# Optimization experiments

Measured on AMD Instinct MI355X. Metric: run time of the kernel, lower is better.

Reference implementation:

```python
import jax, jax.numpy as jnp
import numpy as np

B_SZ, T, H, N, L = 4, 512, 256, 64, 4
EPS = 1e-5

def _hippo(n):
    i = np.arange(n)[:, None]; j = np.arange(n)[None, :]
    A = np.where(i >= j, ((-1.0) ** (i - j)) * np.sqrt((2 * i + 1.0) * (2 * j + 1.0)), 0.0)
    # scale to be contractive so the 512-step dense recurrence stays finite
    A = A / (1.1 * np.linalg.norm(A, 2))
    return A.astype(np.float32)

def _xavier(key, shape):
    fan_in, fan_out = shape[1], shape[0]
    a = float(np.sqrt(6.0 / (fan_in + fan_out)))
    return jax.random.uniform(key, shape, jnp.float32, -a, a)

def setup_inputs() -> dict:
    key = jax.random.key(0)
    ks = jax.random.split(key, 8)
    x = jax.random.normal(ks[0], (B_SZ, T, H), jnp.float32)
    A = jnp.broadcast_to(jnp.asarray(_hippo(N)), (L, N, N))
    Bm = jnp.stack([_xavier(jax.random.fold_in(ks[1], l), (N, H)) for l in range(L)])
    Cm = jnp.stack([_xavier(jax.random.fold_in(ks[2], l), (H, N)) for l in range(L)])
    Dm = jnp.stack([_xavier(jax.random.fold_in(ks[3], l), (H, H)) for l in range(L)])
    Win = _xavier(ks[4], (H, H)); bin_ = jnp.zeros((H,), jnp.float32)
    Wout = _xavier(ks[5], (H, H)); bout = jnp.zeros((H,), jnp.float32)
    return {"x": x, "Win": Win, "bin_": bin_, "Wout": Wout, "bout": bout,
            "A": A, "Bm": Bm, "Cm": Cm, "Dm": Dm}

def _ln(x):
    m = jnp.mean(x, -1, keepdims=True)
    v = jnp.mean((x - m) ** 2, -1, keepdims=True)
    return (x - m) / jnp.sqrt(v + EPS)

def _ssm_layer(h, A, B, C, D):
    # h: (B,T,H); dense state (B,N,H)
    Cbar = C.mean(0)            # mean over output rows (matches C_state.mean(dim=2))
    BT = B.T                    # (H,N)
    DT = D.T                    # (H,H)
    def step(state, u):        # state (B,N,H), u (B,H)
        y = jnp.einsum('bnh,n->bh', state, Cbar) + u @ DT   # output uses pre-update state
        new_state = jnp.einsum('nm,bmh->bnh', A, state) + (u @ BT)[:, :, None]
        return new_state, y
    state0 = jnp.zeros((h.shape[0], A.shape[0], h.shape[2]), h.dtype)
    _, ys = jax.lax.scan(step, state0, jnp.swapaxes(h, 0, 1))  # scan over T
    y = jnp.swapaxes(ys, 0, 1)
    y = jax.nn.gelu(y, approximate=False) + h   # GELU -> (dropout=0) -> residual
    return _ln(y)

def reference(x, Win, bin_, Wout, bout, A, Bm, Cm, Dm):
    h = x @ Win.T + bin_
    for l in range(L):
        h = _ssm_layer(h, A[l], Bm[l], Cm[l], Dm[l])
    h = _ln(h)
    return h @ Wout.T + bout
```

## Files before the change

kernel.cpp:

```cpp
#include <hip/hip_runtime.h>

#define TSEQ 512
#define HDIM 256
#define NDIM 64
#define LC   48
#define MT   16
#define NWB  128

typedef __attribute__((ext_vector_type(4))) float  f32x4;
typedef __attribute__((ext_vector_type(8))) short  s16x8;
typedef __attribute__((ext_vector_type(4))) unsigned short u16x4;
typedef unsigned long long u64;
typedef unsigned short us;

#define MFMA16 __builtin_amdgcn_mfma_f32_16x16x32_bf16

__device__ __forceinline__ float lane_bcast(float v, int l) {
    return __int_as_float(__builtin_amdgcn_readlane(__float_as_int(v), l));
}
__device__ __forceinline__ us f2bf(float f) {
    unsigned u = __float_as_uint(f);
    u += 0x7fffu + ((u >> 16) & 1u);
    return (us)(u >> 16);
}
__device__ __forceinline__ float bf2f(us h) {
    return __uint_as_float(((unsigned)h) << 16);
}
__device__ __forceinline__ int swz(int row, int chunk) {
    return row * 512 + (((chunk) ^ (row & 7)) << 4);
}
__device__ __forceinline__ void st_mall(float* p, float v) {
    __hip_atomic_store(p, v, __ATOMIC_RELAXED, __HIP_MEMORY_SCOPE_AGENT);
}
__device__ __forceinline__ void st_mall8(u64* p, u64 v) {
    __hip_atomic_store(p, v, __ATOMIC_RELAXED, __HIP_MEMORY_SCOPE_AGENT);
}
__device__ __forceinline__ u64 ld_mall8(const u64* p) {
    return __hip_atomic_load(p, __ATOMIC_RELAXED, __HIP_MEMORY_SCOPE_AGENT);
}
__device__ __forceinline__ void flag_set(unsigned* f) {
    __hip_atomic_store(f, 1u, __ATOMIC_RELAXED, __HIP_MEMORY_SCOPE_AGENT);
}
__device__ __forceinline__ void flag_wait(const unsigned* f) {
    while (__hip_atomic_load(f, __ATOMIC_RELAXED, __HIP_MEMORY_SCOPE_AGENT) == 0u)
        __builtin_amdgcn_s_sleep(4);
}

__global__ void __launch_bounds__(512, 2) k_fused(
    const float* __restrict__ x, const float* __restrict__ bin,
    const float* __restrict__ bout, const float* __restrict__ A,
    const float* __restrict__ Bm, const float* __restrict__ Cm,
    const float* __restrict__ Dm, const float* __restrict__ Win,
    const float* __restrict__ Wout,
    us* __restrict__ Win_bf, us* __restrict__ Wout_bf,
    us* __restrict__ Bm_bf, us* __restrict__ Dm_bf,
    float* __restrict__ wbuf, float* __restrict__ BiA, float* __restrict__ BiB,
    unsigned* __restrict__ flags, float* __restrict__ out)
{
    __shared__ __align__(16) char smem[53568];
    us*    xl   = (us*)smem;
    float* yl   = (float*)(smem + 8192);
    float* bwin = (float*)(smem + 24832);
    float* wlds = (float*)(smem + 41216);
    float* cfin = (float*)(smem + 53504);

    const int gid = blockIdx.x, tid = threadIdx.x;
    const int lane = tid & 63, wv = tid >> 6;
    const int m = lane & 15, cgq = lane >> 4;
    const f32x4 z4 = {0.f, 0.f, 0.f, 0.f};
    unsigned* ctr = &flags[516];

    if (gid == NWB) {
        float* As  = (float*)smem;
        float* A8s = (float*)(smem + 16384);
        float* uls = (float*)(smem + 32768);
        float cbv = 0.f;
        if (wv < 4) {
            const float* cp = Cm + (size_t)wv * HDIM * NDIM + lane;
            float s0 = 0.f, s1 = 0.f, s2 = 0.f, s3 = 0.f;
            for (int h = 0; h < HDIM; h += 4) {
                s0 += cp[(h + 0) * NDIM]; s1 += cp[(h + 1) * NDIM];
                s2 += cp[(h + 2) * NDIM]; s3 += cp[(h + 3) * NDIM];
            }
            cbv = ((s0 + s1) + (s2 + s3)) * (1.0f / HDIM);
        } else {
            int t = tid - 256;
            for (int q = t; q < 1024; q += 256) ((f32x4*)As)[q] = ((const f32x4*)A)[q];
        }
        __syncthreads();
        if (wv < 4) {
            float u = cbv;
            uls[(wv * 8 + 0) * 64 + lane] = u;
#pragma unroll 1
            for (int s = 1; s < 8; ++s) {
                float p0 = 0.f, p1 = 0.f, p2 = 0.f, p3 = 0.f;
#pragma unroll
                for (int k = 0; k < 64; k += 4) {
                    p0 += As[(k + 0) * 64 + lane] * lane_bcast(u, k + 0);
                    p1 += As[(k + 1) * 64 + lane] * lane_bcast(u, k + 1);
                    p2 += As[(k + 2) * 64 + lane] * lane_bcast(u, k + 2);
                    p3 += As[(k + 3) * 64 + lane] * lane_bcast(u, k + 3);
                }
                u = (p0 + p1) + (p2 + p3);
                uls[(wv * 8 + s) * 64 + lane] = u;
            }
        } else {
            int t = tid - 256;
            int r = t >> 2, c0 = (t & 3) * 16;
            f32x4 a0 = z4, a1 = z4, a2 = z4, a3 = z4;
            for (int k = 0; k < 64; ++k) {
                float av = As[r * 64 + k];
                const f32x4* bp = (const f32x4*)(As + k * 64 + c0);
                a0 += av * bp[0]; a1 += av * bp[1]; a2 += av * bp[2]; a3 += av * bp[3];
            }
            f32x4* dp = (f32x4*)(A8s + r * 64 + c0);
            dp[0] = a0; dp[1] = a1; dp[2] = a2; dp[3] = a3;
        }
        __syncthreads();
        {
            int r = tid >> 3, c0 = (tid & 7) * 8;
            f32x4 a0 = z4, a1 = z4;
            for (int k = 0; k < 64; ++k) {
                float av = A8s[r * 64 + k];
                const f32x4* bp = (const f32x4*)(A8s + k * 64 + c0);
                a0 += av * bp[0]; a1 += av * bp[1];
            }
            __syncthreads();
            *(f32x4*)(As + r * 64 + c0) = a0;
            *(f32x4*)(As + r * 64 + c0 + 4) = a1;
        }
        __syncthreads();
        {
            int r = tid >> 3, c0 = (tid & 7) * 8;
            f32x4 a0 = z4, a1 = z4;
            for (int k = 0; k < 64; ++k) {
                float av = As[r * 64 + k];
                const f32x4* bp = (const f32x4*)(As + k * 64 + c0);
                a0 += av * bp[0]; a1 += av * bp[1];
            }
            __syncthreads();
            *(f32x4*)(A8s + r * 64 + c0) = a0;
            *(f32x4*)(A8s + r * 64 + c0 + 4) = a1;
        }
        __syncthreads();
        {
            float u = uls[wv * 64 + lane];
#pragma unroll 1
            for (int k6 = 0; k6 < 6; ++k6) {
                st_mall(&wbuf[(size_t)(wv + 8 * k6) * 64 + lane], u);
                if (k6 < 5) {
                    float n0 = 0.f;
#pragma unroll
                    for (int k = 0; k < 64; ++k)
                        n0 += A8s[k * 64 + lane] * lane_bcast(u, k);
                    u = n0;
                }
            }
        }
        __syncthreads();
        if (tid == 0) flag_set(&flags[0]);
        {
            float u1 = uls[(8 + wv) * 64 + lane];
            float u2 = uls[(16 + wv) * 64 + lane];
            float u3 = uls[(24 + wv) * 64 + lane];
#pragma unroll 1
            for (int k6 = 0; k6 < 6; ++k6) {
                const int j = wv + 8 * k6;
                st_mall(&wbuf[(size_t)(1 * LC + j) * 64 + lane], u1);
                st_mall(&wbuf[(size_t)(2 * LC + j) * 64 + lane], u2);
                st_mall(&wbuf[(size_t)(3 * LC + j) * 64 + lane], u3);
                if (k6 < 5) {
                    float n1 = 0.f, n2 = 0.f, n3 = 0.f;
#pragma unroll
                    for (int k = 0; k < 64; ++k) {
                        float a = A8s[k * 64 + lane];
                        n1 += a * lane_bcast(u1, k); n2 += a * lane_bcast(u2, k);
                        n3 += a * lane_bcast(u3, k);
                    }
                    u1 = n1; u2 = n2; u3 = n3;
                }
            }
        }
        __syncthreads();
        if (tid < 3) flag_set(&flags[1 + tid]);
        return;
    }

    const int b = gid >> 5, tb = gid & 31, t0 = tb * MT;
    const size_t grow = (size_t)(b * TSEQ + t0);

    {
        const int base = gid * 896;
        for (int q = base + tid; q < base + 896; q += 512) {
            const float* s; us* d; int off;
            if (q < 16384)      { s = Win;  d = Win_bf;  off = q; }
            else if (q < 32768) { s = Wout; d = Wout_bf; off = q - 16384; }
            else if (q < 49152) { s = Bm;   d = Bm_bf;   off = q - 32768; }
            else                { s = Dm;   d = Dm_bf;   off = q - 49152; }
            f32x4 v = ((const f32x4*)s)[off];
            u64 pk = (u64)f2bf(v[0]) | ((u64)f2bf(v[1]) << 16)
                   | ((u64)f2bf(v[2]) << 32) | ((u64)f2bf(v[3]) << 48);
            st_mall8((u64*)d + off, pk);
        }
    }
    {
        const f32x4* gs = (const f32x4*)(x + grow * HDIM);
#pragma unroll
        for (int k = 0; k < 2; ++k) {
            int q = tid + k * 512;
            int row = q >> 6, c4 = q & 63;
            f32x4 v = gs[q];
            u16x4 pk; pk[0] = f2bf(v[0]); pk[1] = f2bf(v[1]); pk[2] = f2bf(v[2]); pk[3] = f2bf(v[3]);
            *(u16x4*)((char*)xl + swz(row, c4 >> 1) + (c4 & 1) * 8) = pk;
        }
    }
    __syncthreads();
    if (tid == 0) {
        __hip_atomic_fetch_add(ctr, 1u, __ATOMIC_RELAXED, __HIP_MEMORY_SCOPE_AGENT);
        while (__hip_atomic_load(ctr, __ATOMIC_RELAXED, __HIP_MEMORY_SCOPE_AGENT) < 128u)
            __builtin_amdgcn_s_sleep(4);
    }
    __syncthreads();

    {
        f32x4 accA = z4, accB = z4;
        const us* W0 = Win_bf + (size_t)(wv * 32 + m) * HDIM;
        const us* W1 = W0 + (size_t)16 * HDIM;
#pragma unroll
        for (int ks = 0; ks < 8; ++ks) {
            s16x8 av = *(const s16x8*)((const char*)xl + swz(m, ks * 4 + cgq));
            s16x8 b0 = *(const s16x8*)(W0 + ks * 32 + cgq * 8);
            s16x8 b1 = *(const s16x8*)(W1 + ks * 32 + cgq * 8);
            accA = MFMA16(av, b0, accA, 0, 0, 0);
            accB = MFMA16(av, b1, accB, 0, 0, 0);
        }
        __syncthreads();
        const int h0c = wv * 32 + m, h1c = h0c + 16;
        float bi0 = bin[h0c], bi1 = bin[h1c];
#pragma unroll
        for (int reg = 0; reg < 4; ++reg) {
            int trow = cgq * 4 + reg;
            *(us*)((char*)xl + swz(trow, h0c >> 3) + (h0c & 7) * 2) = f2bf(accA[reg] + bi0);
            *(us*)((char*)xl + swz(trow, h1c >> 3) + (h1c & 7) * 2) = f2bf(accB[reg] + bi1);
        }
    }
    __syncthreads();

    if (wv < 4) {
        f32x4 accb = z4;
        const us* B0 = Bm_bf + (size_t)(wv * 16 + m) * HDIM;
#pragma unroll
        for (int ks = 0; ks < 8; ++ks) {
            s16x8 av = *(const s16x8*)((const char*)xl + swz(m, ks * 4 + cgq));
            s16x8 bv = *(const s16x8*)(B0 + ks * 32 + cgq * 8);
            accb = MFMA16(av, bv, accb, 0, 0, 0);
        }
#pragma unroll
        for (int reg = 0; reg < 4; ++reg)
            st_mall(&BiA[(grow + cgq * 4 + reg) * NDIM + wv * 16 + m], accb[reg]);
    }
    __syncthreads();
    if (tid == 0) flag_set(&flags[4 + 0 * NWB + gid]);

#pragma unroll 1
    for (int l = 0; l < 4; ++l) {
        const us* Dl = Dm_bf + (size_t)l * HDIM * HDIM;
        const float* bi = (l & 1) ? BiB : BiA;
        float*       bo = (l & 1) ? BiA : BiB;

        f32x4 accA = z4, accB = z4;
        {
            const us* D0 = Dl + (size_t)(wv * 32 + m) * HDIM;
            const us* D1 = D0 + (size_t)16 * HDIM;
#pragma unroll
            for (int ks = 0; ks < 8; ++ks) {
                s16x8 av = *(const s16x8*)((const char*)xl + swz(m, ks * 4 + cgq));
                s16x8 b0 = *(const s16x8*)(D0 + ks * 32 + cgq * 8);
                s16x8 b1 = *(const s16x8*)(D1 + ks * 32 + cgq * 8);
                accA = MFMA16(av, b0, accA, 0, 0, 0);
                accB = MFMA16(av, b1, accB, 0, 0, 0);
            }
        }

        if (tid == 0) {
            flag_wait(&flags[l]);
#pragma unroll
            for (int nb = 1; nb <= 3; ++nb)
                if (tb - nb >= 0) flag_wait(&flags[4 + l * NWB + gid - nb]);
        }
        __syncthreads();

        {
            const u64* ws8 = (const u64*)(wbuf + (size_t)l * LC * NDIM);
            for (int q = tid; q < LC * NDIM / 2; q += 512)
                ((u64*)wlds)[q] = ld_mall8(&ws8[q]);
            const u64* bi8 = (const u64*)(bi + (size_t)b * TSEQ * NDIM);
#pragma unroll
            for (int k = 0; k < 4; ++k) {
                int q = tid + k * 512;
                int r = q >> 5, cc = q & 31;
                int t = t0 - LC + r;
                ((u64*)bwin)[q] = (t >= 0) ? ld_mall8(&bi8[(size_t)t * 32 + cc]) : 0ull;
            }
        }
        __syncthreads();

        {
            const int r0 = wv * 2;
            float c0 = 0.f, c1 = 0.f;
            float v0 = bwin[(LC - 1 + r0) * NDIM + lane];
            float v1 = bwin[(LC + r0) * NDIM + lane];
#pragma unroll
            for (int j = 0; j < LC; ++j) {
                float wj = wlds[j * NDIM + lane];
                c0 += wj * v0; c1 += wj * v1;
                v1 = v0;
                int nr = LC - 2 + r0 - j; nr = nr < 0 ? 0 : nr;
                v0 = bwin[nr * NDIM + lane];
            }
#pragma unroll
            for (int k = 1; k < 64; k <<= 1) {
                c0 += __shfl_xor(c0, k, 64); c1 += __shfl_xor(c1, k, 64);
            }
            if (lane == 0) { cfin[r0] = c0; cfin[r0 + 1] = c1; }
        }
        __syncthreads();

#pragma unroll
        for (int nt = 0; nt < 2; ++nt) {
            int hcol = wv * 32 + nt * 16 + m;
#pragma unroll
            for (int reg = 0; reg < 4; ++reg) {
                int trow = cgq * 4 + reg;
                float val = (nt ? accB[reg] : accA[reg]) + cfin[trow];
                float g = 0.5f * val * (1.0f + erff(val * 0.70710678118654752f));
                float r = bf2f(*(const us*)((const char*)xl + swz(trow, hcol >> 3) + (hcol & 7) * 2));
                yl[trow * 260 + hcol] = g + r;
            }
        }
        __syncthreads();

        {
            const bool last = (l == 3);
#pragma unroll
            for (int q = 0; q < 2; ++q) {
                int r = wv * 2 + q;
                f32x4 yv = *(const f32x4*)(yl + r * 260 + lane * 4);
                float s = (yv[0] + yv[1]) + (yv[2] + yv[3]);
                float sq = yv[0] * yv[0] + yv[1] * yv[1] + yv[2] * yv[2] + yv[3] * yv[3];
#pragma unroll
                for (int k = 1; k < 64; k <<= 1) {
                    s += __shfl_xor(s, k, 64); sq += __shfl_xor(sq, k, 64);
                }
                float mn = s * (1.0f / HDIM);
                float var = sq * (1.0f / HDIM) - mn * mn;
                float rs = rsqrtf(var + 1e-5f);
                if (last) { float vz = var * rs * rs; rs = rs * rsqrtf(vz + 1e-5f); }
                u16x4 zp;
                zp[0] = f2bf((yv[0] - mn) * rs); zp[1] = f2bf((yv[1] - mn) * rs);
                zp[2] = f2bf((yv[2] - mn) * rs); zp[3] = f2bf((yv[3] - mn) * rs);
                *(u16x4*)((char*)xl + swz(r, lane >> 1) + (lane & 1) * 8) = zp;
            }
        }
        __syncthreads();

        if (l < 3) {
            if (wv < 4) {
                f32x4 accb = z4;
                const us* B0 = Bm_bf + (size_t)(l + 1) * NDIM * HDIM + (size_t)(wv * 16 + m) * HDIM;
#pragma unroll
                for (int ks = 0; ks < 8; ++ks) {
                    s16x8 av = *(const s16x8*)((const char*)xl + swz(m, ks * 4 + cgq));
                    s16x8 bv = *(const s16x8*)(B0 + ks * 32 + cgq * 8);
                    accb = MFMA16(av, bv, accb, 0, 0, 0);
                }
#pragma unroll
                for (int reg = 0; reg < 4; ++reg)
                    st_mall(&bo[(grow + cgq * 4 + reg) * NDIM + wv * 16 + m], accb[reg]);
            }
            __syncthreads();
            if (tid == 0) flag_set(&flags[4 + (l + 1) * NWB + gid]);
        } else {
            f32x4 a2A = z4, a2B = z4;
            const us* W0 = Wout_bf + (size_t)(wv * 32 + m) * HDIM;
            const us* W1 = W0 + (size_t)16 * HDIM;
#pragma unroll
            for (int ks = 0; ks < 8; ++ks) {
                s16x8 av = *(const s16x8*)((const char*)xl + swz(m, ks * 4 + cgq));
                s16x8 b0 = *(const s16x8*)(W0 + ks * 32 + cgq * 8);
                s16x8 b1 = *(const s16x8*)(W1 + ks * 32 + cgq * 8);
                a2A = MFMA16(av, b0, a2A, 0, 0, 0);
                a2B = MFMA16(av, b1, a2B, 0, 0, 0);
            }
#pragma unroll
            for (int nt = 0; nt < 2; ++nt) {
                int hcol = wv * 32 + nt * 16 + m;
                float bo2 = bout[hcol];
#pragma unroll
                for (int reg = 0; reg < 4; ++reg) {
                    int trow = cgq * 4 + reg;
                    out[(grow + trow) * HDIM + hcol] = (nt ? a2B[reg] : a2A[reg]) + bo2;
                }
            }
        }
    }
}

extern "C" void kernel_launch(void* const* d_in, const int* in_sizes, int n_in,
                              void* d_out, int out_size, void* d_ws, size_t ws_size,
                              hipStream_t stream) {
    (void)in_sizes; (void)n_in; (void)out_size; (void)ws_size;
    const float* x    = (const float*)d_in[0];
    const float* Win  = (const float*)d_in[1];
    const float* bin  = (const float*)d_in[2];
    const float* Wout = (const float*)d_in[3];
    const float* bout = (const float*)d_in[4];
    const float* A    = (const float*)d_in[5];
    const float* Bm   = (const float*)d_in[6];
    const float* Cm   = (const float*)d_in[7];
    const float* Dm   = (const float*)d_in[8];

    float* ws     = (float*)d_ws;
    float* wbuf   = ws;
    float* biA    = ws + 21504;
    float* biB    = ws + 152576;
    unsigned* flags = (unsigned*)(ws + 283648);
    us* Win_bf  = (us*)(ws + 284672);
    us* Wout_bf = Win_bf + 65536;
    us* Bm_bf   = Wout_bf + 65536;
    us* Dm_bf   = Bm_bf + 65536;
    float* out  = (float*)d_out;

    hipMemsetAsync(flags, 0, 520 * sizeof(unsigned), stream);
    k_fused<<<NWB + 1, 512, 0, stream>>>(x, bin, bout, A, Bm, Cm, Dm, Win, Wout,
                                         Win_bf, Wout_bf, Bm_bf, Dm_bf,
                                         wbuf, biA, biB, flags, out);
}
```

Measured before the change: 71.74 us.

## Offload weight bf16 conversion to dedicated blocks with per-segment readiness counters

Adds 28 extra blocks whose only job is converting Win, Bm, each layer's Dm and Wout to bf16. Each weight segment gets its own completion counter. Worker blocks no longer do conversion or wait on a 128-block grid barrier. They wait only for Win/Bm/Dm0 before the input projection, and for each later layer's Dm (or Wout) just before that layer needs it. The aim is to take the conversion off the critical path and overlap it with early compute, at the cost of more blocks and more flag polling.

```diff
diff --git a/kernel.cpp b/kernel.cpp
--- a/kernel.cpp
+++ b/kernel.cpp
@@ -6,6 +6,7 @@
 #define LC   48
 #define MT   16
 #define NWB  128
+#define CTR0 516
 
 typedef __attribute__((ext_vector_type(4))) float  f32x4;
 typedef __attribute__((ext_vector_type(8))) short  s16x8;
@@ -43,6 +44,10 @@
 }
 __device__ __forceinline__ void flag_wait(const unsigned* f) {
     while (__hip_atomic_load(f, __ATOMIC_RELAXED, __HIP_MEMORY_SCOPE_AGENT) == 0u)
+        __builtin_amdgcn_s_sleep(4);
+}
+__device__ __forceinline__ void ctr_wait(const unsigned* f, unsigned n) {
+    while (__hip_atomic_load(f, __ATOMIC_RELAXED, __HIP_MEMORY_SCOPE_AGENT) < n)
         __builtin_amdgcn_s_sleep(4);
 }
 
@@ -68,7 +73,31 @@
     const int lane = tid & 63, wv = tid >> 6;
     const int m = lane & 15, cgq = lane >> 4;
     const f32x4 z4 = {0.f, 0.f, 0.f, 0.f};
-    unsigned* ctr = &flags[516];
+
+    if (gid > NWB) {
+        const int cb = gid - (NWB + 1);
+        const int seg = cb >> 2, sub = cb & 3;
+        const float* src; us* dst;
+        if (seg == 0)      { src = Win;  dst = Win_bf; }
+        else if (seg == 1) { src = Bm;   dst = Bm_bf; }
+        else if (seg <= 5) { src = Dm + (size_t)(seg - 2) * 65536;
+                             dst = Dm_bf + (size_t)(seg - 2) * 65536; }
+        else               { src = Wout; dst = Wout_bf; }
+        const int base = sub * 4096;
+#pragma unroll
+        for (int i = 0; i < 8; ++i) {
+            int q = base + tid + i * 512;
+            f32x4 v = ((const f32x4*)src)[q];
+            u64 pk = (u64)f2bf(v[0]) | ((u64)f2bf(v[1]) << 16)
+                   | ((u64)f2bf(v[2]) << 32) | ((u64)f2bf(v[3]) << 48);
+            st_mall8((u64*)dst + q, pk);
+        }
+        __syncthreads();
+        if (tid == 0)
+            __hip_atomic_fetch_add(&flags[CTR0 + seg], 1u,
+                                   __ATOMIC_RELAXED, __HIP_MEMORY_SCOPE_AGENT);
+        return;
+    }
 
     if (gid == NWB) {
         float* As  = (float*)smem;
@@ -190,20 +219,6 @@
     const size_t grow = (size_t)(b * TSEQ + t0);
 
     {
-        const int base = gid * 896;
-        for (int q = base + tid; q < base + 896; q += 512) {
-            const float* s; us* d; int off;
-            if (q < 16384)      { s = Win;  d = Win_bf;  off = q; }
-            else if (q < 32768) { s = Wout; d = Wout_bf; off = q - 16384; }
-            else if (q < 49152) { s = Bm;   d = Bm_bf;   off = q - 32768; }
-            else                { s = Dm;   d = Dm_bf;   off = q - 49152; }
-            f32x4 v = ((const f32x4*)s)[off];
-            u64 pk = (u64)f2bf(v[0]) | ((u64)f2bf(v[1]) << 16)
-                   | ((u64)f2bf(v[2]) << 32) | ((u64)f2bf(v[3]) << 48);
-            st_mall8((u64*)d + off, pk);
-        }
-    }
-    {
         const f32x4* gs = (const f32x4*)(x + grow * HDIM);
 #pragma unroll
         for (int k = 0; k < 2; ++k) {
@@ -216,9 +231,9 @@
     }
     __syncthreads();
     if (tid == 0) {
-        __hip_atomic_fetch_add(ctr, 1u, __ATOMIC_RELAXED, __HIP_MEMORY_SCOPE_AGENT);
-        while (__hip_atomic_load(ctr, __ATOMIC_RELAXED, __HIP_MEMORY_SCOPE_AGENT) < 128u)
-            __builtin_amdgcn_s_sleep(4);
+        ctr_wait(&flags[CTR0 + 0], 4u);
+        ctr_wait(&flags[CTR0 + 1], 4u);
+        ctr_wait(&flags[CTR0 + 2], 4u);
     }
     __syncthreads();
 
@@ -287,6 +302,8 @@
 #pragma unroll
             for (int nb = 1; nb <= 3; ++nb)
                 if (tb - nb >= 0) flag_wait(&flags[4 + l * NWB + gid - nb]);
+            if (l < 3) ctr_wait(&flags[CTR0 + 3 + l], 4u);
+            else       ctr_wait(&flags[CTR0 + 6], 4u);
         }
         __syncthreads();
 
@@ -431,8 +448,8 @@
     us* Dm_bf   = Bm_bf + 65536;
     float* out  = (float*)d_out;
 
-    hipMemsetAsync(flags, 0, 520 * sizeof(unsigned), stream);
-    k_fused<<<NWB + 1, 512, 0, stream>>>(x, bin, bout, A, Bm, Cm, Dm, Win, Wout,
-                                         Win_bf, Wout_bf, Bm_bf, Dm_bf,
-                                         wbuf, biA, biB, flags, out);
-}
+    hipMemsetAsync(flags, 0, 524 * sizeof(unsigned), stream);
+    k_fused<<<NWB + 1 + 28, 512, 0, stream>>>(x, bin, bout, A, Bm, Cm, Dm, Win, Wout,
+                                              Win_bf, Wout_bf, Bm_bf, Dm_bf,
+                                              wbuf, biA, biB, flags, out);
+}
```

Result: faster. 68.88 us (-4.0%).
